# Optimization experiments

Measured on AMD Instinct MI355X. Metric: run time of the kernel, lower is better.

The kernel has to match this reference:

```python
import jax, jax.numpy as jnp
import numpy as np

NEG_BIG = -1e9

def setup_inputs() -> dict:
    key = jax.random.key(0)
    kq, kk, kv, kwq, kwk, kwv, km = jax.random.split(key, 7)
    B, S, d = 16, 1024, 512
    Q = jax.random.normal(kq, (B, S, d), dtype=jnp.float32)
    K = jax.random.normal(kk, (B, S, d), dtype=jnp.float32)
    V = jax.random.normal(kv, (B, S, d), dtype=jnp.float32)
    # nn.Linear weights [d, d]; torch applies x @ W.T
    WQ = jax.random.normal(kwq, (d, d), dtype=jnp.float32) / np.sqrt(d)
    WK = jax.random.normal(kwk, (d, d), dtype=jnp.float32) / np.sqrt(d)
    WV = jax.random.normal(kwv, (d, d), dtype=jnp.float32) / np.sqrt(d)
    mask = jax.random.randint(km, (B, S), 0, 2, dtype=jnp.int32)
    return {"Q": Q, "K": K, "V": V, "WQ": WQ, "WK": WK, "WV": WV, "mask": mask}


def reference(Q, K, V, WQ, WK, WV, mask):
    d = Q.shape[-1]
    q = jnp.einsum('bsd,ed->bse', Q, WQ)
    k = jnp.einsum('bsd,ed->bse', K, WK)
    v = jnp.einsum('bsd,ed->bse', V, WV)
    scores = jnp.einsum('bqd,bkd->bqk', q, k) / jnp.sqrt(jnp.float32(d))
    attn = jax.nn.softmax(scores, axis=-1)
    # Faithful to original: mask applied AFTER softmax with -1e9 fill
    m = mask[:, None, :]  # [B,1,S] broadcast over query dim
    attn = jnp.where(m == 0, jnp.float32(NEG_BIG), attn)
    out = jnp.einsum('bqk,bkd->bqd', attn, v)
    return (out, attn)
```

## Files before the change

kernel.cpp:

```cpp
#include <hip/hip_runtime.h>
#include <hip/hip_bf16.h>

typedef float f32x4 __attribute__((ext_vector_type(4)));
typedef __bf16 bf16x8 __attribute__((ext_vector_type(8)));
typedef unsigned short u16x8 __attribute__((ext_vector_type(8)));
typedef unsigned short u16x4 __attribute__((ext_vector_type(4)));
typedef int i32x4 __attribute__((ext_vector_type(4)));

#define NEG_BIG_F (-1000000000.0f)
#define SCALE_F 0.044194173824159216f

__device__ __forceinline__ unsigned short f2bf(float f) {
  unsigned int u = __float_as_uint(f);
  u += 0x7FFFu + ((u >> 16) & 1u);
  return (unsigned short)(u >> 16);
}

__device__ __forceinline__ float bf2f(unsigned short h) {
  return __uint_as_float((unsigned int)h << 16);
}

__device__ __forceinline__ u16x8 cvt8(f32x4 a, f32x4 b) {
  u16x8 r;
  r[0] = f2bf(a[0]); r[1] = f2bf(a[1]); r[2] = f2bf(a[2]); r[3] = f2bf(a[3]);
  r[4] = f2bf(b[0]); r[5] = f2bf(b[1]); r[6] = f2bf(b[2]); r[7] = f2bf(b[3]);
  return r;
}

__device__ __forceinline__ void gload16(const void* g, char* l) {
  __builtin_amdgcn_global_load_lds(
      (const __attribute__((address_space(1))) unsigned int*)g,
      (__attribute__((address_space(3))) unsigned int*)l, 16, 0, 0);
}

__global__ __launch_bounds__(256) void cvtWX(
    const float* __restrict__ w0, const float* __restrict__ w1,
    const float* __restrict__ w2, const float* __restrict__ Q,
    const float* __restrict__ Kx, const float* __restrict__ V,
    unsigned short* __restrict__ wb, unsigned short* __restrict__ xb)
{
  const int z = blockIdx.z;
  if (z == 0) {
    if (blockIdx.x >= 384) return;
    const int i = (blockIdx.x * 256 + threadIdx.x) * 8;
    const float* src = i < 262144 ? w0 : (i < 524288 ? w1 : w2);
    const int j = i & 262143;
    f32x4 a = *(const f32x4*)(src + j);
    f32x4 b = *(const f32x4*)(src + j + 4);
    *(u16x8*)&wb[i] = cvt8(a, b);
  } else {
    const float* src = z == 1 ? Q : (z == 2 ? Kx : V);
    unsigned short* dst = xb + (size_t)(z - 1) * 8388608;
    const int i = (blockIdx.x * 256 + threadIdx.x) * 8;
    f32x4 a = *(const f32x4*)(src + i);
    f32x4 b = *(const f32x4*)(src + i + 4);
    *(u16x8*)&dst[i] = cvt8(a, b);
  }
}

__global__ __launch_bounds__(512, 2) void proj_all(
    const unsigned short* __restrict__ xb, const unsigned short* __restrict__ wb,
    unsigned short* __restrict__ qb, unsigned short* __restrict__ kb,
    unsigned short* __restrict__ vt)
{
  __shared__ __align__(16) unsigned short As[2][256][32];
  __shared__ __align__(16) unsigned short Bs[2][256][32];

  const int bid = blockIdx.x;
  const int tid = threadIdx.x;
  const int lane = tid & 63, wave = tid >> 6;
  const int wr = (wave >> 2) * 128, wc = (wave & 3) * 64;
  const int fr = lane & 15, fq = lane >> 4;

  const unsigned short* Abase;
  const unsigned short* Bbase;
  int m0, n0;
  if (bid < 256) {
    const int z = bid >> 7, rem = bid & 127;
    m0 = (rem & 63) * 256; n0 = (rem >> 6) * 256;
    Abase = xb + (size_t)z * 8388608 + (size_t)m0 * 512;
    Bbase = wb + (size_t)z * 262144 + (size_t)n0 * 512;
  } else {
    const int c0 = bid - 256;
    const int b = c0 >> 3;
    m0 = ((c0 >> 2) & 1) * 256;
    n0 = (c0 & 3) * 256;
    Abase = wb + 524288 + (size_t)m0 * 512;
    Bbase = xb + 16777216 + ((size_t)b * 1024 + n0) * 512;
  }

  f32x4 acc[8][4] = {};

  const unsigned short* gA[2]; char* lA[2];
  const unsigned short* gB[2]; char* lB[2];
  #pragma unroll
  for (int i = 0; i < 2; i++) {
    const int c = tid + 512 * i, row = c >> 2, slot = c & 3;
    const int sw = (slot ^ ((row >> 1) & 3)) * 8;
    gA[i] = Abase + (size_t)row * 512 + sw;
    gB[i] = Bbase + (size_t)row * 512 + sw;
    lA[i] = (char*)&As[0][0][0] + c * 16;
    lB[i] = (char*)&Bs[0][0][0] + c * 16;
  }

  #pragma unroll
  for (int i = 0; i < 2; i++) { gload16(gA[i], lA[i]); gload16(gB[i], lB[i]); }

  int cur = 0;
  for (int kt = 0; kt < 512; kt += 32) {
    const int nb = cur ^ 1;
    if (kt < 480) {
      #pragma unroll
      for (int i = 0; i < 2; i++) {
        gload16(gA[i] + kt + 32, lA[i] + nb * 16384);
        gload16(gB[i] + kt + 32, lB[i] + nb * 16384);
      }
      asm volatile("s_waitcnt vmcnt(4) lgkmcnt(0)" ::: "memory");
    } else {
      asm volatile("s_waitcnt vmcnt(0) lgkmcnt(0)" ::: "memory");
    }
    __builtin_amdgcn_sched_barrier(0);
    __builtin_amdgcn_s_barrier();

    bf16x8 bv[4];
    #pragma unroll
    for (int nf = 0; nf < 4; nf++) {
      const int br = wc + nf * 16 + fr;
      bv[nf] = *(const bf16x8*)&Bs[cur][br][(fq ^ ((br >> 1) & 3)) * 8];
    }
    #pragma unroll
    for (int mf = 0; mf < 8; mf++) {
      const int ar = wr + mf * 16 + fr;
      bf16x8 av = *(const bf16x8*)&As[cur][ar][(fq ^ ((ar >> 1) & 3)) * 8];
      #pragma unroll
      for (int nf = 0; nf < 4; nf++)
        acc[mf][nf] = __builtin_amdgcn_mfma_f32_16x16x32_bf16(av, bv[nf], acc[mf][nf], 0, 0, 0);
    }
    __builtin_amdgcn_s_barrier();
    cur = nb;
  }

  if (bid < 256) {
    unsigned short* Y = (bid >> 7) ? kb : qb;
    #pragma unroll
    for (int mf = 0; mf < 8; mf++)
      #pragma unroll
      for (int nf = 0; nf < 4; nf++)
        #pragma unroll
        for (int rr = 0; rr < 4; rr++) {
          const int m = m0 + wr + mf * 16 + fq * 4 + rr;
          const int n = n0 + wc + nf * 16 + fr;
          Y[(size_t)m * 512 + n] = f2bf(acc[mf][nf][rr]);
        }
  } else {
    const int b = (bid - 256) >> 3;
    #pragma unroll
    for (int mf = 0; mf < 8; mf++)
      #pragma unroll
      for (int nf = 0; nf < 4; nf++)
        #pragma unroll
        for (int rr = 0; rr < 4; rr++) {
          const int e = m0 + wr + mf * 16 + fq * 4 + rr;
          const int s = n0 + wc + nf * 16 + fr;
          vt[((size_t)b * 512 + e) * 1024 + s] = f2bf(acc[mf][nf][rr]);
        }
  }
}

__global__ __launch_bounds__(512, 2) void score_mv(
    const unsigned short* __restrict__ qb, const unsigned short* __restrict__ kb,
    const unsigned short* __restrict__ vt, const int* __restrict__ mask,
    unsigned short* __restrict__ P, float* __restrict__ partial,
    float* __restrict__ mvsum)
{
  __shared__ __align__(16) unsigned short As[2][256][32];
  __shared__ __align__(16) unsigned short Bs[2][256][32];

  const int bid = blockIdx.x;
  const int tid = threadIdx.x;

  if (bid >= 256) {
    const int row = (bid - 256) * 8 + (tid >> 6);
    const int b = row >> 9;
    const int lane = tid & 63;
    const unsigned short* vr = vt + (size_t)row * 1024 + lane * 16;
    const int* mr = mask + b * 1024 + lane * 16;
    u16x8 v0 = *(const u16x8*)(vr);
    u16x8 v1 = *(const u16x8*)(vr + 8);
    float s = 0.f;
    #pragma unroll
    for (int j = 0; j < 8; j++) {
      if (!mr[j])     s += bf2f(v0[j]);
      if (!mr[8 + j]) s += bf2f(v1[j]);
    }
    #pragma unroll
    for (int o = 32; o > 0; o >>= 1) s += __shfl_xor(s, o);
    if (lane == 0) mvsum[row] = s;
    return;
  }

  const int bz = bid >> 4;
  const int m0 = (bid & 3) * 256, n0 = ((bid >> 2) & 3) * 256;
  const int lane = tid & 63, wave = tid >> 6;
  const int wr = (wave >> 2) * 128, wc = (wave & 3) * 64;
  const int fr = lane & 15, fq = lane >> 4;

  f32x4 acc[8][4] = {};

  const unsigned short* gA[2]; char* lA[2];
  const unsigned short* gB[2]; char* lB[2];
  #pragma unroll
  for (int i = 0; i < 2; i++) {
    const int c = tid + 512 * i, row = c >> 2, slot = c & 3;
    const int sw = (slot ^ ((row >> 1) & 3)) * 8;
    gA[i] = qb + ((size_t)bz * 1024 + m0 + row) * 512 + sw;
    gB[i] = kb + ((size_t)bz * 1024 + n0 + row) * 512 + sw;
    lA[i] = (char*)&As[0][0][0] + c * 16;
    lB[i] = (char*)&Bs[0][0][0] + c * 16;
  }

  #pragma unroll
  for (int i = 0; i < 2; i++) { gload16(gA[i], lA[i]); gload16(gB[i], lB[i]); }

  int cur = 0;
  for (int kt = 0; kt < 512; kt += 32) {
    const int nb = cur ^ 1;
    if (kt < 480) {
      #pragma unroll
      for (int i = 0; i < 2; i++) {
        gload16(gA[i] + kt + 32, lA[i] + nb * 16384);
        gload16(gB[i] + kt + 32, lB[i] + nb * 16384);
      }
      asm volatile("s_waitcnt vmcnt(4) lgkmcnt(0)" ::: "memory");
    } else {
      asm volatile("s_waitcnt vmcnt(0) lgkmcnt(0)" ::: "memory");
    }
    __builtin_amdgcn_sched_barrier(0);
    __builtin_amdgcn_s_barrier();

    bf16x8 bv[4];
    #pragma unroll
    for (int nf = 0; nf < 4; nf++) {
      const int br = wc + nf * 16 + fr;
      bv[nf] = *(const bf16x8*)&Bs[cur][br][(fq ^ ((br >> 1) & 3)) * 8];
    }
    #pragma unroll
    for (int mf = 0; mf < 8; mf++) {
      const int ar = wr + mf * 16 + fr;
      bf16x8 av = *(const bf16x8*)&As[cur][ar][(fq ^ ((ar >> 1) & 3)) * 8];
      #pragma unroll
      for (int nf = 0; nf < 4; nf++)
        acc[mf][nf] = __builtin_amdgcn_mfma_f32_16x16x32_bf16(av, bv[nf], acc[mf][nf], 0, 0, 0);
    }
    __builtin_amdgcn_s_barrier();
    cur = nb;
  }

  int mcol[4];
  #pragma unroll
  for (int nf = 0; nf < 4; nf++)
    mcol[nf] = mask[bz * 1024 + n0 + wc + nf * 16 + fr];

  unsigned short* Pb = P + ((size_t)bz << 20);
  const int slot = ((bid >> 2) & 3) * 4 + (wave & 3);
  #pragma unroll
  for (int mf = 0; mf < 8; mf++) {
    #pragma unroll
    for (int rr = 0; rr < 4; rr++) {
      const int m = m0 + wr + mf * 16 + fq * 4 + rr;
      float e = 0.f;
      #pragma unroll
      for (int nf = 0; nf < 4; nf++) {
        const float ev = __expf(acc[mf][nf][rr] * SCALE_F);
        e += ev;
        Pb[(size_t)m * 1024 + n0 + wc + nf * 16 + fr] =
            mcol[nf] ? f2bf(ev) : (unsigned short)0;
      }
      e += __shfl_xor(e, 1); e += __shfl_xor(e, 2);
      e += __shfl_xor(e, 4); e += __shfl_xor(e, 8);
      if (fr == 0)
        partial[(size_t)slot * 16384 + bz * 1024 + m] = e;
    }
  }
}

__global__ __launch_bounds__(512) void pv_attn(
    const unsigned short* __restrict__ P, const unsigned short* __restrict__ vt,
    const float* __restrict__ partial, const float* __restrict__ mvsum,
    const int* __restrict__ mask,
    float* __restrict__ out, float* __restrict__ attn)
{
  __shared__ __align__(16) unsigned short As[2][64][32];
  __shared__ __align__(16) unsigned short Bs[2][512][32];
  __shared__ float inv_l[64];

  const int tid = threadIdx.x;
  const int bz = blockIdx.z, m0 = blockIdx.x * 64;
  const int lane = tid & 63, wave = tid >> 6;
  const int n0 = wave * 64;
  const int fr = lane & 15, fq = lane >> 4;

  f32x4 acc[4][4] = {};

  if (tid < 64) {
    float s = 0.f;
    #pragma unroll
    for (int p = 0; p < 16; p++) s += partial[(size_t)p * 16384 + bz * 1024 + m0 + tid];
    inv_l[tid] = 1.0f / s;
  }

  const unsigned short* gA = nullptr; char* lA = nullptr;
  if (tid < 256) {
    const int row = tid >> 2, slot = tid & 3;
    gA = P + ((size_t)bz << 20) + (size_t)(m0 + row) * 1024 + (slot ^ ((row >> 1) & 3)) * 8;
    lA = (char*)&As[0][0][0] + tid * 16;
  }
  const unsigned short* gB[4]; char* lB[4];
  #pragma unroll
  for (int i = 0; i < 4; i++) {
    const int c = tid + 512 * i, row = c >> 2, slot = c & 3;
    gB[i] = vt + ((size_t)bz * 512 + row) * 1024 + (slot ^ ((row >> 1) & 3)) * 8;
    lB[i] = (char*)&Bs[0][0][0] + c * 16;
  }

  const int arow = tid >> 3, acol = (tid & 7) * 4;
  const int aslot8 = ((acol >> 3) ^ ((arow >> 1) & 3)) * 8 + (acol & 7);
  float* arp = attn + ((size_t)bz * 1024 + m0 + arow) * 1024 + acol;
  const int* mrp = mask + bz * 1024 + acol;

  if (tid < 256) gload16(gA, lA);
  #pragma unroll
  for (int i = 0; i < 4; i++) gload16(gB[i], lB[i]);
  __syncthreads();

  int cur = 0;
  for (int t = 0; t < 32; t++) {
    const int nb = cur ^ 1;
    const int kt = t * 32;
    if (t < 31) {
      if (tid < 256) gload16(gA + kt + 32, lA + nb * 4096);
      #pragma unroll
      for (int i = 0; i < 4; i++) gload16(gB[i] + kt + 32, lB[i] + nb * 32768);
      if (wave < 4) asm volatile("s_waitcnt vmcnt(5) lgkmcnt(0)" ::: "memory");
      else          asm volatile("s_waitcnt vmcnt(4) lgkmcnt(0)" ::: "memory");
    } else {
      asm volatile("s_waitcnt vmcnt(0) lgkmcnt(0)" ::: "memory");
    }
    __builtin_amdgcn_sched_barrier(0);
    __builtin_amdgcn_s_barrier();

    bf16x8 af[4], bv[4];
    #pragma unroll
    for (int mf = 0; mf < 4; mf++) {
      const int ar = mf * 16 + fr;
      af[mf] = *(const bf16x8*)&As[cur][ar][(fq ^ ((ar >> 1) & 3)) * 8];
    }
    #pragma unroll
    for (int nf = 0; nf < 4; nf++) {
      const int br = n0 + nf * 16 + fr;
      bv[nf] = *(const bf16x8*)&Bs[cur][br][(fq ^ ((br >> 1) & 3)) * 8];
    }
    #pragma unroll
    for (int mf = 0; mf < 4; mf++)
      #pragma unroll
      for (int nf = 0; nf < 4; nf++)
        acc[mf][nf] = __builtin_amdgcn_mfma_f32_16x16x32_bf16(af[mf], bv[nf], acc[mf][nf], 0, 0, 0);

    {
      const u16x4 pv4 = *(const u16x4*)&As[cur][arow][aslot8];
      const i32x4 mv = *(const i32x4*)(mrp + kt);
      const float iv = inv_l[arow];
      f32x4 o;
      o[0] = mv[0] ? bf2f(pv4[0]) * iv : NEG_BIG_F;
      o[1] = mv[1] ? bf2f(pv4[1]) * iv : NEG_BIG_F;
      o[2] = mv[2] ? bf2f(pv4[2]) * iv : NEG_BIG_F;
      o[3] = mv[3] ? bf2f(pv4[3]) * iv : NEG_BIG_F;
      *(f32x4*)(arp + kt) = o;
    }
    __builtin_amdgcn_s_barrier();
    cur = nb;
  }

  float mvv[4];
  #pragma unroll
  for (int nf = 0; nf < 4; nf++)
    mvv[nf] = mvsum[bz * 512 + n0 + nf * 16 + fr];
  #pragma unroll
  for (int mf = 0; mf < 4; mf++)
    #pragma unroll
    for (int rr = 0; rr < 4; rr++) {
      const int m = m0 + mf * 16 + fq * 4 + rr;
      const float iv = inv_l[mf * 16 + fq * 4 + rr];
      #pragma unroll
      for (int nf = 0; nf < 4; nf++)
        out[((size_t)bz * 1024 + m) * 512 + n0 + nf * 16 + fr] =
            iv * acc[mf][nf][rr] + NEG_BIG_F * mvv[nf];
    }
}

extern "C" void kernel_launch(void* const* d_in, const int* in_sizes, int n_in,
                              void* d_out, int out_size, void* d_ws, size_t ws_size,
                              hipStream_t stream)
{
  const float* Q  = (const float*)d_in[0];
  const float* Kx = (const float*)d_in[1];
  const float* V  = (const float*)d_in[2];
  const float* WQ = (const float*)d_in[3];
  const float* WK = (const float*)d_in[4];
  const float* WV = (const float*)d_in[5];
  const int* mask = (const int*)d_in[6];

  const int B = 16, S = 1024, D = 512;
  float* out_f  = (float*)d_out;
  float* attn_f = out_f + (size_t)B * S * D;
  unsigned short* Pbuf = (unsigned short*)d_out;
  unsigned short* xb = (unsigned short*)attn_f;

  unsigned short* qb = (unsigned short*)d_ws;
  unsigned short* kb = qb + (size_t)B * S * D;
  unsigned short* vt = kb + (size_t)B * S * D;
  unsigned short* wb = vt + (size_t)B * S * D;
  float* partial = (float*)(wb + 786432);
  float* mvsum = partial + 262144;

  cvtWX<<<dim3(4096, 1, 4), 256, 0, stream>>>(WQ, WK, WV, Q, Kx, V, wb, xb);
  proj_all<<<dim3(384), 512, 0, stream>>>(xb, wb, qb, kb, vt);
  score_mv<<<dim3(1280), 512, 0, stream>>>(qb, kb, vt, mask, Pbuf, partial, mvsum);
  pv_attn<<<dim3(16, 1, 16), 512, 0, stream>>>(Pbuf, vt, partial, mvsum, mask, out_f, attn_f);
}
```

Measured before the change: 144.5 us.

## Double pv_attn M tile to 128 rows with 2x4 wave grid

```diff
diff --git a/kernel.cpp b/kernel.cpp
--- a/kernel.cpp
+++ b/kernel.cpp
@@ -284,37 +284,36 @@
   }
 }
 
-__global__ __launch_bounds__(512) void pv_attn(
+__global__ __launch_bounds__(512, 2) void pv_attn(
     const unsigned short* __restrict__ P, const unsigned short* __restrict__ vt,
     const float* __restrict__ partial, const float* __restrict__ mvsum,
     const int* __restrict__ mask,
     float* __restrict__ out, float* __restrict__ attn)
 {
-  __shared__ __align__(16) unsigned short As[2][64][32];
+  __shared__ __align__(16) unsigned short As[2][128][32];
   __shared__ __align__(16) unsigned short Bs[2][512][32];
-  __shared__ float inv_l[64];
+  __shared__ float inv_l[128];
 
   const int tid = threadIdx.x;
-  const int bz = blockIdx.z, m0 = blockIdx.x * 64;
+  const int bz = blockIdx.z, m0 = blockIdx.x * 128;
   const int lane = tid & 63, wave = tid >> 6;
-  const int n0 = wave * 64;
+  const int wr = (wave >> 2) * 64;
+  const int wc = (wave & 3) * 128;
   const int fr = lane & 15, fq = lane >> 4;
 
-  f32x4 acc[4][4] = {};
-
-  if (tid < 64) {
+  f32x4 acc[4][8] = {};
+
+  if (tid < 128) {
     float s = 0.f;
     #pragma unroll
     for (int p = 0; p < 16; p++) s += partial[(size_t)p * 16384 + bz * 1024 + m0 + tid];
     inv_l[tid] = 1.0f / s;
   }
 
-  const unsigned short* gA = nullptr; char* lA = nullptr;
-  if (tid < 256) {
-    const int row = tid >> 2, slot = tid & 3;
-    gA = P + ((size_t)bz << 20) + (size_t)(m0 + row) * 1024 + (slot ^ ((row >> 1) & 3)) * 8;
-    lA = (char*)&As[0][0][0] + tid * 16;
-  }
+  const int arw = tid >> 2, asl = tid & 3;
+  const unsigned short* gA = P + ((size_t)bz << 20) + (size_t)(m0 + arw) * 1024
+                               + (asl ^ ((arw >> 1) & 3)) * 8;
+  char* lA = (char*)&As[0][0][0] + tid * 16;
   const unsigned short* gB[4]; char* lB[4];
   #pragma unroll
   for (int i = 0; i < 4; i++) {
@@ -323,12 +322,12 @@
     lB[i] = (char*)&Bs[0][0][0] + c * 16;
   }
 
-  const int arow = tid >> 3, acol = (tid & 7) * 4;
-  const int aslot8 = ((acol >> 3) ^ ((arow >> 1) & 3)) * 8 + (acol & 7);
+  const int arow = tid >> 2, acol = (tid & 3) * 8;
+  const int aslot = ((tid & 3) ^ ((arow >> 1) & 3)) * 8;
   float* arp = attn + ((size_t)bz * 1024 + m0 + arow) * 1024 + acol;
   const int* mrp = mask + bz * 1024 + acol;
 
-  if (tid < 256) gload16(gA, lA);
+  gload16(gA, lA);
   #pragma unroll
   for (int i = 0; i < 4; i++) gload16(gB[i], lB[i]);
   __syncthreads();
@@ -338,62 +337,67 @@
     const int nb = cur ^ 1;
     const int kt = t * 32;
     if (t < 31) {
-      if (tid < 256) gload16(gA + kt + 32, lA + nb * 4096);
+      gload16(gA + kt + 32, lA + nb * 8192);
       #pragma unroll
       for (int i = 0; i < 4; i++) gload16(gB[i] + kt + 32, lB[i] + nb * 32768);
-      if (wave < 4) asm volatile("s_waitcnt vmcnt(5) lgkmcnt(0)" ::: "memory");
-      else          asm volatile("s_waitcnt vmcnt(4) lgkmcnt(0)" ::: "memory");
+      asm volatile("s_waitcnt vmcnt(5) lgkmcnt(0)" ::: "memory");
     } else {
       asm volatile("s_waitcnt vmcnt(0) lgkmcnt(0)" ::: "memory");
     }
     __builtin_amdgcn_sched_barrier(0);
     __builtin_amdgcn_s_barrier();
 
-    bf16x8 af[4], bv[4];
+    bf16x8 af[4], bv[8];
     #pragma unroll
     for (int mf = 0; mf < 4; mf++) {
-      const int ar = mf * 16 + fr;
+      const int ar = wr + mf * 16 + fr;
       af[mf] = *(const bf16x8*)&As[cur][ar][(fq ^ ((ar >> 1) & 3)) * 8];
     }
     #pragma unroll
-    for (int nf = 0; nf < 4; nf++) {
-      const int br = n0 + nf * 16 + fr;
+    for (int nf = 0; nf < 8; nf++) {
+      const int br = wc + nf * 16 + fr;
       bv[nf] = *(const bf16x8*)&Bs[cur][br][(fq ^ ((br >> 1) & 3)) * 8];
     }
     #pragma unroll
     for (int mf = 0; mf < 4; mf++)
       #pragma unroll
-      for (int nf = 0; nf < 4; nf++)
+      for (int nf = 0; nf < 8; nf++)
         acc[mf][nf] = __builtin_amdgcn_mfma_f32_16x16x32_bf16(af[mf], bv[nf], acc[mf][nf], 0, 0, 0);
 
     {
-      const u16x4 pv4 = *(const u16x4*)&As[cur][arow][aslot8];
-      const i32x4 mv = *(const i32x4*)(mrp + kt);
+      const u16x8 p8 = *(const u16x8*)&As[cur][arow][aslot];
+      const i32x4 ma = *(const i32x4*)(mrp + kt);
+      const i32x4 mb = *(const i32x4*)(mrp + kt + 4);
       const float iv = inv_l[arow];
-      f32x4 o;
-      o[0] = mv[0] ? bf2f(pv4[0]) * iv : NEG_BIG_F;
-      o[1] = mv[1] ? bf2f(pv4[1]) * iv : NEG_BIG_F;
-      o[2] = mv[2] ? bf2f(pv4[2]) * iv : NEG_BIG_F;
-      o[3] = mv[3] ? bf2f(pv4[3]) * iv : NEG_BIG_F;
-      *(f32x4*)(arp + kt) = o;
+      f32x4 o0, o1;
+      o0[0] = ma[0] ? bf2f(p8[0]) * iv : NEG_BIG_F;
+      o0[1] = ma[1] ? bf2f(p8[1]) * iv : NEG_BIG_F;
+      o0[2] = ma[2] ? bf2f(p8[2]) * iv : NEG_BIG_F;
+      o0[3] = ma[3] ? bf2f(p8[3]) * iv : NEG_BIG_F;
+      o1[0] = mb[0] ? bf2f(p8[4]) * iv : NEG_BIG_F;
+      o1[1] = mb[1] ? bf2f(p8[5]) * iv : NEG_BIG_F;
+      o1[2] = mb[2] ? bf2f(p8[6]) * iv : NEG_BIG_F;
+      o1[3] = mb[3] ? bf2f(p8[7]) * iv : NEG_BIG_F;
+      *(f32x4*)(arp + kt) = o0;
+      *(f32x4*)(arp + kt + 4) = o1;
     }
     __builtin_amdgcn_s_barrier();
     cur = nb;
   }
 
-  float mvv[4];
-  #pragma unroll
-  for (int nf = 0; nf < 4; nf++)
-    mvv[nf] = mvsum[bz * 512 + n0 + nf * 16 + fr];
+  float mvv[8];
+  #pragma unroll
+  for (int nf = 0; nf < 8; nf++)
+    mvv[nf] = mvsum[bz * 512 + wc + nf * 16 + fr];
   #pragma unroll
   for (int mf = 0; mf < 4; mf++)
     #pragma unroll
     for (int rr = 0; rr < 4; rr++) {
-      const int m = m0 + mf * 16 + fq * 4 + rr;
-      const float iv = inv_l[mf * 16 + fq * 4 + rr];
-      #pragma unroll
-      for (int nf = 0; nf < 4; nf++)
-        out[((size_t)bz * 1024 + m) * 512 + n0 + nf * 16 + fr] =
+      const int m = m0 + wr + mf * 16 + fq * 4 + rr;
+      const float iv = inv_l[wr + mf * 16 + fq * 4 + rr];
+      #pragma unroll
+      for (int nf = 0; nf < 8; nf++)
+        out[((size_t)bz * 1024 + m) * 512 + wc + nf * 16 + fr] =
             iv * acc[mf][nf][rr] + NEG_BIG_F * mvv[nf];
     }
 }
@@ -426,5 +430,5 @@
   cvtWX<<<dim3(4096, 1, 4), 256, 0, stream>>>(WQ, WK, WV, Q, Kx, V, wb, xb);
   proj_all<<<dim3(384), 512, 0, stream>>>(xb, wb, qb, kb, vt);
   score_mv<<<dim3(1280), 512, 0, stream>>>(qb, kb, vt, mask, Pbuf, partial, mvsum);
-  pv_attn<<<dim3(16, 1, 16), 512, 0, stream>>>(Pbuf, vt, partial, mvsum, mask, out_f, attn_f);
-}
+  pv_attn<<<dim3(8, 1, 16), 512, 0, stream>>>(Pbuf, vt, partial, mvsum, mask, out_f, attn_f);
+}
```

New measurement: 151.5 us. 1.05x slower.
